# Performance work log

Measured on AMD Instinct MI355X. Metric: run time of the kernel, lower is better.

## Reference

```python
import jax, jax.numpy as jnp
import numpy as np

EMBED = 1024
HEADS = 16
HEAD_DIM = EMBED // HEADS  # 64 quantum wires


def setup_inputs() -> dict:
    key = jax.random.key(0)
    ks = jax.random.split(key, 6)
    s = 1.0 / np.sqrt(EMBED)
    return {
        "x": jax.random.normal(ks[0], (8, 4096, EMBED), dtype=jnp.float32),
        "Wk": jax.random.normal(ks[1], (EMBED, EMBED), dtype=jnp.float32) * s,
        "Wq": jax.random.normal(ks[2], (EMBED, EMBED), dtype=jnp.float32) * s,
        "Wv": jax.random.normal(ks[3], (EMBED, EMBED), dtype=jnp.float32) * s,
        "Wo": jax.random.normal(ks[4], (EMBED, EMBED), dtype=jnp.float32) * s,
        "theta": jax.random.normal(ks[5], (HEAD_DIM,), dtype=jnp.float32),
    }


def reference(x, Wk, Wq, Wv, Wo, theta):
    b, s, _ = x.shape
    # linear projections (torch Linear: y = x @ W^T), split heads -> [b,s,h,d]
    def proj(W):
        return (x @ W.T).reshape(b, s, HEADS, HEAD_DIM)
    k, q, v = proj(Wk), proj(Wq), proj(Wv)
    # QLayer: per-wire RX(x_i) then trainable RX(theta_i) on |0>, measure PauliZ
    # -> <Z_i> = cos(x_i + theta_i) exactly (product state, independent wires).
    k_q = jnp.cos(k + theta)
    q_q = jnp.cos(q + theta)
    v_q = jnp.cos(v + theta)
    # Faithful to source: matmul over last two dims of [b,s,h,d] -> attention
    # across the HEADS axis ([b,s,h,h]), not across sequence.
    scores = jnp.einsum('bsid,bsjd->bsij', q_q, k_q) / jnp.sqrt(
        jnp.asarray(HEAD_DIM, dtype=x.dtype))
    attn = jax.nn.softmax(scores, axis=-1)  # dropout = identity at inference
    out = jnp.einsum('bsij,bsjd->bsid', attn, v_q).reshape(b, s, EMBED)
    return out @ Wo.T
```

## Files before the change

### kernel.cpp

```cpp
#include <hip/hip_runtime.h>
#include <hip/hip_fp16.h>

#define NTOK 32768
#define NE   1024

typedef _Float16 half_t;
typedef _Float16 f16x8 __attribute__((ext_vector_type(8)));
typedef _Float16 f16x4 __attribute__((ext_vector_type(4)));
typedef float    f32x4 __attribute__((ext_vector_type(4)));

typedef __attribute__((address_space(1))) const unsigned int guint;
typedef __attribute__((address_space(3))) unsigned int luint;

__device__ __forceinline__ void async16(const void* g, void* l) {
    __builtin_amdgcn_global_load_lds((guint*)g, (luint*)l, 16, 0, 0);
}

__global__ __launch_bounds__(256) void cvt_f32_f16(const float* __restrict__ s,
                                                   half_t* __restrict__ d, int n) {
    int i = (blockIdx.x * 256 + threadIdx.x) * 8;
    if (i >= n) return;
    float4 a = *(const float4*)(s + i);
    float4 b = *(const float4*)(s + i + 4);
    f16x8 h = {(_Float16)a.x, (_Float16)a.y, (_Float16)a.z, (_Float16)a.w,
               (_Float16)b.x, (_Float16)b.y, (_Float16)b.z, (_Float16)b.w};
    *(f16x8*)(d + i) = h;
}

template <bool QKV>
__global__ __launch_bounds__(256) void gemm_bt(const half_t* __restrict__ A,
                                               const half_t* __restrict__ Bbase,
                                               void* __restrict__ Cout,
                                               const float* __restrict__ theta) {
    constexpr int K = 1024;
    constexpr int J = QKV ? 24 : 8;
    __shared__ alignas(16) half_t As[128 * 64];
    __shared__ alignas(16) half_t Bs[128 * 64];

    const int id   = blockIdx.x;
    const int xcd  = id & 7;
    const int slot = id >> 3;
    const int ygrp = slot / J;
    const int j    = slot - ygrp * J;
    const int ytile = ygrp * 8 + xcd;
    const int zsl  = QKV ? (j >> 3) : 0;
    const int xt   = j & 7;

    const int tid  = threadIdx.x;
    const int wave = tid >> 6;
    const int lane = tid & 63;
    const int quad = lane >> 4;
    const int l16  = lane & 15;
    const int sw   = l16 & 7;
    const int wr   = wave >> 1, wc = wave & 1;
    const size_t m0 = (size_t)ytile * 128;
    const int    n0 = xt * 128;

    const half_t* Bp = Bbase + (size_t)zsl * (size_t)(NE * NE);
    const half_t* Ag = A + m0 * K;
    const half_t* Bg = Bp + (size_t)n0 * K;

    const int ar = tid >> 3;
    const int ac = ((tid & 7) ^ (ar & 7)) * 8;

    f32x4 acc[4][4];
#pragma unroll
    for (int i = 0; i < 4; ++i)
#pragma unroll
        for (int jj = 0; jj < 4; ++jj) acc[i][jj] = (f32x4){0.f, 0.f, 0.f, 0.f};

    for (int k0 = 0; k0 < K; k0 += 64) {
#pragma unroll
        for (int i = 0; i < 4; ++i)
            async16(Ag + (size_t)(i * 32 + ar) * K + (k0 + ac),
                    (char*)As + (i * 256 + wave * 64) * 16);
#pragma unroll
        for (int i = 0; i < 4; ++i)
            async16(Bg + (size_t)(i * 32 + ar) * K + (k0 + ac),
                    (char*)Bs + (i * 256 + wave * 64) * 16);
        __syncthreads();

#pragma unroll
        for (int kk = 0; kk < 64; kk += 32) {
            f16x8 af[4], bf[4];
#pragma unroll
            for (int t = 0; t < 4; ++t) {
                const int swz = (((kk >> 3) + quad) ^ sw) * 8;
                af[t] = *(const f16x8*)&As[(wr * 64 + t * 16 + l16) * 64 + swz];
                bf[t] = *(const f16x8*)&Bs[(wc * 64 + t * 16 + l16) * 64 + swz];
            }
#pragma unroll
            for (int mt = 0; mt < 4; ++mt)
#pragma unroll
                for (int nt = 0; nt < 4; ++nt)
                    acc[mt][nt] = __builtin_amdgcn_mfma_f32_16x16x32_f16(
                        af[mt], bf[nt], acc[mt][nt], 0, 0, 0);
        }
        __syncthreads();
    }

    if (QKV) {
        half_t* C = (half_t*)Cout + (size_t)zsl * ((size_t)NTOK * NE);
#pragma unroll
        for (int nt = 0; nt < 4; ++nt) {
            const int n = n0 + wc * 64 + nt * 16 + l16;
            const float th = theta[n & 63];
#pragma unroll
            for (int mt = 0; mt < 4; ++mt) {
                const size_t mb = m0 + wr * 64 + mt * 16 + quad * 4;
#pragma unroll
                for (int r = 0; r < 4; ++r)
                    C[(mb + r) * NE + n] = (half_t)__cosf(acc[mt][nt][r] + th);
            }
        }
    } else {
        float* C = (float*)Cout;
#pragma unroll
        for (int nt = 0; nt < 4; ++nt) {
            const int n = n0 + wc * 64 + nt * 16 + l16;
#pragma unroll
            for (int mt = 0; mt < 4; ++mt) {
                const size_t mb = m0 + wr * 64 + mt * 16 + quad * 4;
#pragma unroll
                for (int r = 0; r < 4; ++r) C[(mb + r) * NE + n] = acc[mt][nt][r];
            }
        }
    }
}

__global__ __launch_bounds__(256) void attn_kernel(const half_t* __restrict__ q,
                                                   const half_t* __restrict__ k,
                                                   const half_t* __restrict__ v,
                                                   half_t* __restrict__ out) {
    __shared__ half_t vT[4][64][20];
    __shared__ half_t Pl[4][16][20];
    const int tid  = threadIdx.x;
    const int w    = tid >> 6;
    const int lane = tid & 63;
    const int quad = lane >> 4;
    const int l16  = lane & 15;
    const size_t base = ((size_t)blockIdx.x * 4 + w) * 1024;

    {
        const int h = lane >> 2, d0 = (lane & 3) * 16;
        f16x8 va = *(const f16x8*)(v + base + h * 64 + d0);
        f16x8 vb = *(const f16x8*)(v + base + h * 64 + d0 + 8);
#pragma unroll
        for (int z = 0; z < 8; ++z) {
            vT[w][d0 + z][h]     = va[z];
            vT[w][d0 + 8 + z][h] = vb[z];
        }
    }

    f16x8 aq0 = *(const f16x8*)(q + base + l16 * 64 + quad * 8);
    f16x8 aq1 = *(const f16x8*)(q + base + l16 * 64 + 32 + quad * 8);
    f16x8 bk0 = *(const f16x8*)(k + base + l16 * 64 + quad * 8);
    f16x8 bk1 = *(const f16x8*)(k + base + l16 * 64 + 32 + quad * 8);
    f32x4 S = __builtin_amdgcn_mfma_f32_16x16x32_f16(aq0, bk0, (f32x4){0.f,0.f,0.f,0.f}, 0, 0, 0);
    S = __builtin_amdgcn_mfma_f32_16x16x32_f16(aq1, bk1, S, 0, 0, 0);

#pragma unroll
    for (int r = 0; r < 4; ++r) {
        float s = S[r] * 0.125f;
        float mx = s;
#pragma unroll
        for (int o = 8; o; o >>= 1) mx = fmaxf(mx, __shfl_xor(mx, o));
        float e = __expf(s - mx);
        float sum = e;
#pragma unroll
        for (int o = 8; o; o >>= 1) sum += __shfl_xor(sum, o);
        Pl[w][quad * 4 + r][l16] = (half_t)(e / sum);
    }
    __syncthreads();

    f16x4 ap = *(const f16x4*)&Pl[w][l16][quad * 4];
#pragma unroll
    for (int c = 0; c < 4; ++c) {
        f16x4 bv = *(const f16x4*)&vT[w][c * 16 + l16][quad * 4];
        f32x4 O = __builtin_amdgcn_mfma_f32_16x16x16f16(ap, bv, (f32x4){0.f,0.f,0.f,0.f}, 0, 0, 0);
#pragma unroll
        for (int r = 0; r < 4; ++r)
            out[base + (quad * 4 + r) * 64 + c * 16 + l16] = (half_t)O[r];
    }
}

extern "C" void kernel_launch(void* const* d_in, const int* in_sizes, int n_in,
                              void* d_out, int out_size, void* d_ws, size_t ws_size,
                              hipStream_t stream) {
    const float* x     = (const float*)d_in[0];
    const float* Wk    = (const float*)d_in[1];
    const float* Wq    = (const float*)d_in[2];
    const float* Wv    = (const float*)d_in[3];
    const float* Wo    = (const float*)d_in[4];
    const float* theta = (const float*)d_in[5];

    char* ws = (char*)d_ws;
    half_t* xh  = (half_t*)ws;
    half_t* wh  = (half_t*)(ws + (size_t)(64 << 20));
    half_t* qkv = (half_t*)(ws + (size_t)(72 << 20));

    cvt_f32_f16<<<NTOK * NE / 2048, 256, 0, stream>>>(x, xh, NTOK * NE);
    cvt_f32_f16<<<NE * NE / 2048, 256, 0, stream>>>(Wq, wh + 0 * NE * NE, NE * NE);
    cvt_f32_f16<<<NE * NE / 2048, 256, 0, stream>>>(Wk, wh + 1 * NE * NE, NE * NE);
    cvt_f32_f16<<<NE * NE / 2048, 256, 0, stream>>>(Wv, wh + 2 * NE * NE, NE * NE);
    cvt_f32_f16<<<NE * NE / 2048, 256, 0, stream>>>(Wo, wh + 3 * NE * NE, NE * NE);

    gemm_bt<true><<<6144, 256, 0, stream>>>(xh, wh, qkv, theta);

    attn_kernel<<<NTOK / 4, 256, 0, stream>>>(qkv, qkv + (size_t)NTOK * NE,
                                              qkv + 2 * (size_t)NTOK * NE, xh);

    gemm_bt<false><<<2048, 256, 0, stream>>>(xh, wh + 3 * NE * NE, d_out, nullptr);
}
```

Baseline: 645.0 us.

## Rewrite GEMM with 256x256 tiles, 8 waves, double-buffered async LDS pipeline

The GEMM kernel moves from 128x128 tiles with 4 waves and a single LDS buffer to 256x256 tiles with 8 waves. Operand staging is split into quarter-tiles and double buffered, using explicit vmcnt waits and barriers so global-to-LDS loads overlap the MFMA work. MFMA blocks also get raised scheduling priority. The aim is higher arithmetic intensity per block and hidden memory latency, at the cost of 64KB of LDS, more registers per thread, and fewer blocks in the grid.

```diff
diff --git a/kernel.cpp b/kernel.cpp
--- a/kernel.cpp
+++ b/kernel.cpp
@@ -27,76 +27,151 @@
     *(f16x8*)(d + i) = h;
 }
 
+
+#define WAITV(N) asm volatile("s_waitcnt vmcnt(" #N ")" ::: "memory")
+#define BARRIER()                              \
+    do {                                       \
+        asm volatile("" ::: "memory");         \
+        __builtin_amdgcn_s_barrier();          \
+        asm volatile("" ::: "memory");         \
+    } while (0)
+
+#define STAGE_A(dst, q, k0)                                                   \
+    do {                                                                      \
+        _Pragma("unroll") for (int l = 0; l < 2; ++l)                         \
+            async16(Ag + (size_t)(l * 128 + (q) * 64 + rr) * K + (k0) + cc,   \
+                    (char*)(dst) + l * 8192 + w * 1024);                      \
+    } while (0)
+
+#define STAGE_B(dst, r, k0)                                                   \
+    do {                                                                      \
+        _Pragma("unroll") for (int l = 0; l < 2; ++l)                         \
+            async16(Bg + (size_t)((l * 2 + wb) * 64 + (r) * 32 + (rr & 31)) * K + \
+                        (k0) + cc,                                            \
+                    (char*)(dst) + l * 8192 + w * 1024);                      \
+    } while (0)
+
+#define READ_A(dstf, q)                                                       \
+    do {                                                                      \
+        _Pragma("unroll") for (int i = 0; i < 4; ++i)                         \
+        _Pragma("unroll") for (int x = 0; x < 2; ++x)                         \
+            dstf[i][x] = *(const f16x8*)&As[cur][q][(wr * 64 + i * 16 + l16) * 64 + \
+                                                    (((x * 4 + quad) ^ sw) * 8)]; \
+    } while (0)
+
+#define READ_B(dstf, r)                                                       \
+    do {                                                                      \
+        _Pragma("unroll") for (int i2 = 0; i2 < 2; ++i2)                      \
+        _Pragma("unroll") for (int x = 0; x < 2; ++x)                         \
+            dstf[i2][x] = *(const f16x8*)&Bs[cur][r][(wc * 32 + i2 * 16 + l16) * 64 + \
+                                                     (((x * 4 + quad) ^ sw) * 8)]; \
+    } while (0)
+
+#define MMA(af, bf, QA, RB)                                                   \
+    do {                                                                      \
+        __builtin_amdgcn_s_setprio(1);                                        \
+        _Pragma("unroll") for (int i = 0; i < 4; ++i)                         \
+        _Pragma("unroll") for (int jj = 0; jj < 2; ++jj)                      \
+        _Pragma("unroll") for (int x = 0; x < 2; ++x)                         \
+            acc[(QA) * 4 + i][(RB) * 2 + jj] =                                \
+                __builtin_amdgcn_mfma_f32_16x16x32_f16(                       \
+                    af[i][x], bf[jj][x], acc[(QA) * 4 + i][(RB) * 2 + jj], 0, 0, 0); \
+        __builtin_amdgcn_s_setprio(0);                                        \
+    } while (0)
+
 template <bool QKV>
-__global__ __launch_bounds__(256) void gemm_bt(const half_t* __restrict__ A,
-                                               const half_t* __restrict__ Bbase,
-                                               void* __restrict__ Cout,
-                                               const float* __restrict__ theta) {
-    constexpr int K = 1024;
-    constexpr int J = QKV ? 24 : 8;
-    __shared__ alignas(16) half_t As[128 * 64];
-    __shared__ alignas(16) half_t Bs[128 * 64];
-
-    const int id   = blockIdx.x;
-    const int xcd  = id & 7;
-    const int slot = id >> 3;
-    const int ygrp = slot / J;
-    const int j    = slot - ygrp * J;
-    const int ytile = ygrp * 8 + xcd;
-    const int zsl  = QKV ? (j >> 3) : 0;
-    const int xt   = j & 7;
+__global__ __launch_bounds__(512, 2) void gemm_bt(const half_t* __restrict__ A,
+                                                  const half_t* __restrict__ Bbase,
+                                                  void* __restrict__ Cout,
+                                                  const float* __restrict__ theta) {
+    constexpr int K  = 1024;
+    constexpr int NT = 16;
+    constexpr int J  = QKV ? 12 : 4;
+    __shared__ alignas(16) half_t As[2][2][128 * 64];
+    __shared__ alignas(16) half_t Bs[2][2][128 * 64];
+
+    const int id    = blockIdx.x;
+    const int xcd   = id & 7;
+    const int slot  = id >> 3;
+    const int ygrp  = slot / J;
+    const int j     = slot - ygrp * J;
+    const int mtile = ygrp * 8 + xcd;
+    const int zsl   = QKV ? (j >> 2) : 0;
+    const int xt    = QKV ? (j & 3) : j;
 
     const int tid  = threadIdx.x;
-    const int wave = tid >> 6;
+    const int w    = tid >> 6;
     const int lane = tid & 63;
     const int quad = lane >> 4;
     const int l16  = lane & 15;
     const int sw   = l16 & 7;
-    const int wr   = wave >> 1, wc = wave & 1;
-    const size_t m0 = (size_t)ytile * 128;
-    const int    n0 = xt * 128;
-
-    const half_t* Bp = Bbase + (size_t)zsl * (size_t)(NE * NE);
+    const int wr   = w >> 2, wc = w & 3;
+    const size_t m0 = (size_t)mtile * 256;
+    const int    n0 = xt * 256;
+
     const half_t* Ag = A + m0 * K;
-    const half_t* Bg = Bp + (size_t)n0 * K;
-
-    const int ar = tid >> 3;
-    const int ac = ((tid & 7) ^ (ar & 7)) * 8;
-
-    f32x4 acc[4][4];
-#pragma unroll
-    for (int i = 0; i < 4; ++i)
+    const half_t* Bg = Bbase + (size_t)zsl * (size_t)(NE * NE) + (size_t)n0 * K;
+
+    const int rr = tid >> 3;
+    const int cc = ((tid & 7) ^ (rr & 7)) * 8;
+    const int wb = tid >> 8;
+
+    f32x4 acc[8][4];
+#pragma unroll
+    for (int i = 0; i < 8; ++i)
 #pragma unroll
         for (int jj = 0; jj < 4; ++jj) acc[i][jj] = (f32x4){0.f, 0.f, 0.f, 0.f};
 
-    for (int k0 = 0; k0 < K; k0 += 64) {
-#pragma unroll
-        for (int i = 0; i < 4; ++i)
-            async16(Ag + (size_t)(i * 32 + ar) * K + (k0 + ac),
-                    (char*)As + (i * 256 + wave * 64) * 16);
-#pragma unroll
-        for (int i = 0; i < 4; ++i)
-            async16(Bg + (size_t)(i * 32 + ar) * K + (k0 + ac),
-                    (char*)Bs + (i * 256 + wave * 64) * 16);
-        __syncthreads();
-
-#pragma unroll
-        for (int kk = 0; kk < 64; kk += 32) {
-            f16x8 af[4], bf[4];
-#pragma unroll
-            for (int t = 0; t < 4; ++t) {
-                const int swz = (((kk >> 3) + quad) ^ sw) * 8;
-                af[t] = *(const f16x8*)&As[(wr * 64 + t * 16 + l16) * 64 + swz];
-                bf[t] = *(const f16x8*)&Bs[(wc * 64 + t * 16 + l16) * 64 + swz];
-            }
-#pragma unroll
-            for (int mt = 0; mt < 4; ++mt)
-#pragma unroll
-                for (int nt = 0; nt < 4; ++nt)
-                    acc[mt][nt] = __builtin_amdgcn_mfma_f32_16x16x32_f16(
-                        af[mt], bf[nt], acc[mt][nt], 0, 0, 0);
-        }
-        __syncthreads();
+    STAGE_A(As[0][0], 0, 0);
+    STAGE_B(Bs[0][0], 0, 0);
+    STAGE_B(Bs[0][1], 1, 0);
+    STAGE_A(As[0][1], 1, 0);
+    STAGE_A(As[1][0], 0, 64);
+
+    f16x8 aF[4][2], bF0[2][2], bF1[2][2];
+
+    for (int t = 0; t < NT - 1; ++t) {
+        const int cur = t & 1, nxt = cur ^ 1;
+        const int kn = (t + 1) * 64;
+        WAITV(6);
+        BARRIER();
+        STAGE_B(Bs[nxt][0], 0, kn);
+        READ_A(aF, 0);
+        READ_B(bF0, 0);
+        MMA(aF, bF0, 0, 0);
+        WAITV(6);
+        BARRIER();
+        STAGE_B(Bs[nxt][1], 1, kn);
+        READ_B(bF1, 1);
+        MMA(aF, bF1, 0, 1);
+        WAITV(6);
+        BARRIER();
+        STAGE_A(As[nxt][1], 1, kn);
+        READ_A(aF, 1);
+        MMA(aF, bF1, 1, 1);
+        WAITV(6);
+        BARRIER();
+        if (t + 2 < NT) STAGE_A(As[cur][0], 0, kn + 64);
+        READ_B(bF0, 0);
+        MMA(aF, bF0, 1, 0);
+    }
+    {
+        const int cur = (NT - 1) & 1;
+        WAITV(4);
+        BARRIER();
+        READ_A(aF, 0);
+        READ_B(bF0, 0);
+        MMA(aF, bF0, 0, 0);
+        WAITV(2);
+        BARRIER();
+        READ_B(bF1, 1);
+        MMA(aF, bF1, 0, 1);
+        WAITV(0);
+        BARRIER();
+        READ_A(aF, 1);
+        MMA(aF, bF1, 1, 1);
+        READ_B(bF0, 0);
+        MMA(aF, bF0, 1, 0);
     }
 
     if (QKV) {
@@ -106,8 +181,8 @@
             const int n = n0 + wc * 64 + nt * 16 + l16;
             const float th = theta[n & 63];
 #pragma unroll
-            for (int mt = 0; mt < 4; ++mt) {
-                const size_t mb = m0 + wr * 64 + mt * 16 + quad * 4;
+            for (int mt = 0; mt < 8; ++mt) {
+                const size_t mb = m0 + wr * 128 + mt * 16 + quad * 4;
 #pragma unroll
                 for (int r = 0; r < 4; ++r)
                     C[(mb + r) * NE + n] = (half_t)__cosf(acc[mt][nt][r] + th);
@@ -119,8 +194,8 @@
         for (int nt = 0; nt < 4; ++nt) {
             const int n = n0 + wc * 64 + nt * 16 + l16;
 #pragma unroll
-            for (int mt = 0; mt < 4; ++mt) {
-                const size_t mb = m0 + wr * 64 + mt * 16 + quad * 4;
+            for (int mt = 0; mt < 8; ++mt) {
+                const size_t mb = m0 + wr * 128 + mt * 16 + quad * 4;
 #pragma unroll
                 for (int r = 0; r < 4; ++r) C[(mb + r) * NE + n] = acc[mt][nt][r];
             }
@@ -205,10 +280,10 @@
     cvt_f32_f16<<<NE * NE / 2048, 256, 0, stream>>>(Wv, wh + 2 * NE * NE, NE * NE);
     cvt_f32_f16<<<NE * NE / 2048, 256, 0, stream>>>(Wo, wh + 3 * NE * NE, NE * NE);
 
-    gemm_bt<true><<<6144, 256, 0, stream>>>(xh, wh, qkv, theta);
+    gemm_bt<true><<<1536, 512, 0, stream>>>(xh, wh, qkv, theta);
 
     attn_kernel<<<NTOK / 4, 256, 0, stream>>>(qkv, qkv + (size_t)NTOK * NE,
                                               qkv + 2 * (size_t)NTOK * NE, xh);
 
-    gemm_bt<false><<<2048, 256, 0, stream>>>(xh, wh + 3 * NE * NE, d_out, nullptr);
-}
+    gemm_bt<false><<<512, 512, 0, stream>>>(xh, wh + 3 * NE * NE, d_out, nullptr);
+}
```

Measured after the change: 653.8 us. No clear change (+1.4%).
